# Performance work log

Hardware: AMD Instinct MI355X
Metric: run time of the kernel (lower is better)

## Reference

```python
import jax, jax.numpy as jnp
import numpy as np

COST_MASK = 5.0
COST_DICE = 5.0
COST_BOX = 5.0
COST_GIOU = 2.0


def point_sample(masks, pts):
    # masks: [N, H, W]; pts: [P, 2] with (x, y) in [0, 1].
    # Matches F.grid_sample(bilinear, align_corners=False, padding_mode='zeros')
    N, H, W = masks.shape
    x = pts[:, 0] * W - 0.5
    y = pts[:, 1] * H - 0.5
    x0 = jnp.floor(x)
    y0 = jnp.floor(y)
    wx = x - x0
    wy = y - y0
    x0i = x0.astype(jnp.int32)
    y0i = y0.astype(jnp.int32)

    def gather(yi, xi):
        valid = ((xi >= 0) & (xi < W) & (yi >= 0) & (yi < H)).astype(masks.dtype)
        v = masks[:, jnp.clip(yi, 0, H - 1), jnp.clip(xi, 0, W - 1)]  # [N, P]
        return v * valid

    v00 = gather(y0i, x0i)
    v01 = gather(y0i, x0i + 1)
    v10 = gather(y0i + 1, x0i)
    v11 = gather(y0i + 1, x0i + 1)
    return (v00 * (1 - wy) * (1 - wx) + v01 * (1 - wy) * wx
            + v10 * wy * (1 - wx) + v11 * wy * wx)  # [N, P]


def box_cxcywh_to_xyxy(b):
    cx, cy, w, h = b[..., 0], b[..., 1], b[..., 2], b[..., 3]
    return jnp.stack([cx - 0.5 * w, cy - 0.5 * h, cx + 0.5 * w, cy + 0.5 * h], axis=-1)


def generalized_box_iou(a, b):
    # a: [Q, 4], b: [T, 4] in xyxy
    area_a = (a[:, 2] - a[:, 0]) * (a[:, 3] - a[:, 1])
    area_b = (b[:, 2] - b[:, 0]) * (b[:, 3] - b[:, 1])
    lt = jnp.maximum(a[:, None, :2], b[None, :, :2])
    rb = jnp.minimum(a[:, None, 2:], b[None, :, 2:])
    wh = jnp.clip(rb - lt, 0.0)
    inter = wh[..., 0] * wh[..., 1]
    union = area_a[:, None] + area_b[None, :] - inter
    iou = inter / union
    lt_e = jnp.minimum(a[:, None, :2], b[None, :, :2])
    rb_e = jnp.maximum(a[:, None, 2:], b[None, :, 2:])
    wh_e = jnp.clip(rb_e - lt_e, 0.0)
    area_e = wh_e[..., 0] * wh_e[..., 1]
    return iou - (area_e - union) / area_e


def _cost_one(out_mask, tgt_mask, out_box, tgt_box, pts):
    om = point_sample(out_mask, pts)  # [Q, P] logits
    tm = point_sample(tgt_mask, pts)  # [T, P] binary targets
    P = om.shape[1]
    # batch_sigmoid_ce_loss: BCE(x,1)=softplus(-x), BCE(x,0)=softplus(x)
    pos = jax.nn.softplus(-om)
    neg = jax.nn.softplus(om)
    cost_mask = (jnp.einsum('qp,tp->qt', pos, tm)
                 + jnp.einsum('qp,tp->qt', neg, 1.0 - tm)) / P
    # batch_dice_loss
    s = jax.nn.sigmoid(om)
    numerator = 2.0 * jnp.einsum('qp,tp->qt', s, tm)
    denominator = s.sum(-1)[:, None] + tm.sum(-1)[None, :]
    cost_dice = 1.0 - (numerator + 1.0) / (denominator + 1.0)
    # box costs
    cost_bbox = jnp.abs(out_box[:, None, :] - tgt_box[None, :, :]).sum(-1)
    cost_giou = -generalized_box_iou(box_cxcywh_to_xyxy(out_box),
                                     box_cxcywh_to_xyxy(tgt_box))
    return (COST_MASK * cost_mask + COST_DICE * cost_dice
            + COST_BOX * cost_bbox + COST_GIOU * cost_giou)


def setup_inputs() -> dict:
    key = jax.random.key(0)
    k1, k2, k3, k4, k5 = jax.random.split(key, 5)
    B, Q, T, H, W, P = 2, 300, 300, 256, 256, 12544
    pred_masks = jax.random.normal(k1, (B, Q, H, W), dtype=jnp.float32)
    tgt_masks = (jax.random.uniform(k2, (B, T, H, W)) > 0.5).astype(jnp.float32)
    u = jax.random.uniform(k3, (B, Q, 4), dtype=jnp.float32)
    pred_boxes = jnp.concatenate([0.2 + 0.6 * u[..., :2], 0.05 + 0.25 * u[..., 2:]], axis=-1)
    v = jax.random.uniform(k4, (B, T, 4), dtype=jnp.float32)
    tgt_boxes = jnp.concatenate([0.2 + 0.6 * v[..., :2], 0.05 + 0.25 * v[..., 2:]], axis=-1)
    point_coords = jax.random.uniform(k5, (B, P, 2), dtype=jnp.float32)
    return {"pred_masks": pred_masks, "tgt_masks": tgt_masks,
            "pred_boxes": pred_boxes, "tgt_boxes": tgt_boxes,
            "point_coords": point_coords}


def reference(pred_masks, tgt_masks, pred_boxes, tgt_boxes, point_coords):
    # Batched cost matrix C: [B, Q, T]
    return jax.vmap(_cost_one)(pred_masks, tgt_masks, pred_boxes, tgt_boxes, point_coords)
```

## Files before the change

kernel.cpp:

```cpp
#include <hip/hip_runtime.h>
#include <hip/hip_bf16.h>
#include <math.h>

#define BB 2
#define QQ 300
#define TT 300
#define HH 256
#define WW 256
#define PP 12544
#define NCHUNK 16
#define NSPLIT 14
#define KSPLIT (PP / NSPLIT)
#define KSTEPS (KSPLIT / 64)

typedef __bf16 bf16_t;
typedef bf16_t bf16x8 __attribute__((ext_vector_type(8)));
typedef float floatx4 __attribute__((ext_vector_type(4)));

__device__ inline void gl_lds16(const void* g, void* l) {
    __builtin_amdgcn_global_load_lds(
        (const __attribute__((address_space(1))) unsigned int*)g,
        (__attribute__((address_space(3))) unsigned int*)l, 16, 0, 0);
}

__global__ __launch_bounds__(256) void prep_kernel(const float* __restrict__ pts,
                                                   int4* __restrict__ off,
                                                   float4* __restrict__ wgt,
                                                   int* __restrict__ bkt) {
    int idx = blockIdx.x * 256 + threadIdx.x;
    if (idx >= BB * PP) return;
    float px = pts[idx * 2 + 0];
    float py = pts[idx * 2 + 1];
    float x = px * WW - 0.5f;
    float y = py * HH - 0.5f;
    float x0f = floorf(x), y0f = floorf(y);
    float wx = x - x0f, wy = y - y0f;
    int x0 = (int)x0f, y0 = (int)y0f;
    int x1 = x0 + 1, y1 = y0 + 1;
    float vx0 = (x0 >= 0 && x0 < WW) ? 1.f : 0.f;
    float vx1 = (x1 >= 0 && x1 < WW) ? 1.f : 0.f;
    float vy0 = (y0 >= 0 && y0 < HH) ? 1.f : 0.f;
    float vy1 = (y1 >= 0 && y1 < HH) ? 1.f : 0.f;
    int cx0 = min(max(x0, 0), WW - 1), cx1 = min(max(x1, 0), WW - 1);
    int cy0 = min(max(y0, 0), HH - 1), cy1 = min(max(y1, 0), HH - 1);
    off[idx] = make_int4(cy0 * WW + cx0, cy0 * WW + cx1, cy1 * WW + cx0, cy1 * WW + cx1);
    wgt[idx] = make_float4((1.f - wy) * (1.f - wx) * vy0 * vx0,
                           (1.f - wy) * wx        * vy0 * vx1,
                           wy        * (1.f - wx) * vy1 * vx0,
                           wy        * wx         * vy1 * vx1);
    bkt[idx] = min(max(y0, 0), HH - 2) >> 4;
}

__global__ __launch_bounds__(1024) void sort_kernel(const int4* __restrict__ off,
                                                    const float4* __restrict__ wgt,
                                                    const int* __restrict__ bkt,
                                                    int4* __restrict__ off_s,
                                                    float4* __restrict__ wgt_s,
                                                    int* __restrict__ cs) {
    int b = blockIdx.x;
    int tid = threadIdx.x;
    __shared__ int hist[NCHUNK];
    __shared__ int base_s[NCHUNK];
    if (tid < NCHUNK) hist[tid] = 0;
    __syncthreads();
    for (int p = tid; p < PP; p += 1024) atomicAdd(&hist[bkt[b * PP + p]], 1);
    __syncthreads();
    if (tid == 0) {
        int run = 0;
        for (int i = 0; i < NCHUNK; ++i) { base_s[i] = run; run += hist[i]; }
    }
    __syncthreads();
    if (tid < NCHUNK + 1) cs[b * (NCHUNK + 1) + tid] = (tid < NCHUNK) ? base_s[tid] : PP;
    __syncthreads();
    for (int p = tid; p < PP; p += 1024) {
        int bp = b * PP + p;
        int pos = atomicAdd(&base_s[bkt[bp]], 1);
        off_s[b * PP + pos] = off[bp];
        wgt_s[b * PP + pos] = wgt[bp];
    }
}

__global__ __launch_bounds__(256) void sample_kernel(
    const float* __restrict__ pred_masks, const float* __restrict__ tgt_masks,
    const int4* __restrict__ off_s, const float4* __restrict__ wgt_s,
    const int* __restrict__ cs_g,
    bf16_t* __restrict__ OM, bf16_t* __restrict__ SM, bf16_t* __restrict__ TM,
    float* __restrict__ RS_SP, float* __restrict__ RS_S, float* __restrict__ RS_T) {
    int b = blockIdx.z;
    int m = blockIdx.x;
    int c = blockIdx.y;
    int tid = threadIdx.x;
    int wave = tid >> 6, lane = tid & 63;
    __shared__ __align__(16) float rows[17 * WW];

    bool is_pred = (m < QQ);
    const float* img;
    bf16_t* row0;
    bf16_t* row1 = nullptr;
    if (is_pred) {
        img  = pred_masks + (size_t)(b * QQ + m) * (HH * WW);
        row0 = OM + (size_t)(b * QQ + m) * PP;
        row1 = SM + (size_t)(b * QQ + m) * PP;
    } else {
        int t = m - QQ;
        img  = tgt_masks + (size_t)(b * TT + t) * (HH * WW);
        row0 = TM + (size_t)(b * TT + t) * PP;
    }

    int base = c * 16;
    int nrows = min(17, HH - base);
    const char* gimg = (const char*)(img + base * WW);
    for (int i = wave; i < nrows; i += 4)
        gl_lds16(gimg + i * 1024 + lane * 16, (char*)rows + i * 1024);
    __syncthreads();

    const int4*  offb = off_s + b * PP;
    const float4* wb  = wgt_s + b * PP;
    const int* cs = cs_g + b * (NCHUNK + 1);
    int boff = base * WW;
    int j1 = cs[c + 1];
    float s0 = 0.f, s1 = 0.f;
    for (int j = cs[c] + tid; j < j1; j += 256) {
        int4 o = offb[j];
        float4 w = wb[j];
        float v = w.x * rows[o.x - boff] + w.y * rows[o.y - boff] +
                  w.z * rows[o.z - boff] + w.w * rows[o.w - boff];
        row0[j] = (bf16_t)v;
        if (is_pred) {
            float e = __expf(-fabsf(v));
            float r = 1.f / (1.f + e);
            float sg = (v >= 0.f) ? r : e * r;
            row1[j] = (bf16_t)sg;
            s0 += fmaxf(v, 0.f) + __logf(1.f + e);
            s1 += sg;
        } else {
            s0 += v;
        }
    }
    for (int o = 32; o > 0; o >>= 1) {
        s0 += __shfl_down(s0, o, 64);
        s1 += __shfl_down(s1, o, 64);
    }
    __shared__ float ra[4], rb[4];
    if (lane == 0) { ra[wave] = s0; rb[wave] = s1; }
    __syncthreads();
    if (tid == 0) {
        float t0 = ra[0] + ra[1] + ra[2] + ra[3];
        float t1 = rb[0] + rb[1] + rb[2] + rb[3];
        if (is_pred) {
            atomicAdd(&RS_SP[b * QQ + m], t0);
            atomicAdd(&RS_S[b * QQ + m], t1);
        } else {
            atomicAdd(&RS_T[b * TT + (m - QQ)], t0);
        }
    }
}

__global__ __launch_bounds__(256) void matmul_kernel(
    const bf16_t* __restrict__ OM, const bf16_t* __restrict__ SM, const bf16_t* __restrict__ TM,
    float* __restrict__ A1P, float* __restrict__ A2P) {
    int b = blockIdx.z / NSPLIT;
    int split = blockIdx.z % NSPLIT;
    int m0 = blockIdx.x * 64;
    int n0 = blockIdx.y * 64;
    int tid = threadIdx.x;
    int wave = tid >> 6, lane = tid & 63;
    int lrow = lane & 15, quad = lane >> 4;

    __shared__ __align__(16) bf16_t lds[3 * 64 * 64];

    int k0 = split * KSPLIT;
    int lr8 = lane >> 3;
    int clog = (lane & 7) ^ lr8;

    const char* gp[6];
    unsigned lofs[6];
#pragma unroll
    for (int jj = 0; jj < 6; ++jj) {
        int L = wave + jj * 4;
        int mat = L >> 3, i = L & 7;
        int rb_ = (mat == 2) ? n0 : m0;
        int row = min(rb_ + i * 8 + lr8, (mat == 2) ? (TT - 1) : (QQ - 1));
        const bf16_t* g = (mat == 0) ? OM + (size_t)b * QQ * PP
                        : (mat == 1) ? SM + (size_t)b * QQ * PP
                                     : TM + (size_t)b * TT * PP;
        gp[jj] = (const char*)(g + (size_t)row * PP + k0) + clog * 16;
        lofs[jj] = mat * 4096 + i * 512;
    }

    floatx4 acc1[4] = {{0.f,0.f,0.f,0.f},{0.f,0.f,0.f,0.f},{0.f,0.f,0.f,0.f},{0.f,0.f,0.f,0.f}};
    floatx4 acc2[4] = {{0.f,0.f,0.f,0.f},{0.f,0.f,0.f,0.f},{0.f,0.f,0.f,0.f},{0.f,0.f,0.f,0.f}};

    int ar = wave * 16 + lrow;
    int arx = ar & 7;
    for (int s = 0; s < KSTEPS; ++s) {
#pragma unroll
        for (int jj = 0; jj < 6; ++jj) {
            gl_lds16(gp[jj], lds + lofs[jj]);
            gp[jj] += 128;
        }
        __syncthreads();
#pragma unroll
        for (int kk8 = 0; kk8 <= 4; kk8 += 4) {
            bf16x8 a1 = *(const bf16x8*)(lds + ar * 64 + (((quad + kk8) ^ arx) << 3));
            bf16x8 a2 = *(const bf16x8*)(lds + 4096 + ar * 64 + (((quad + kk8) ^ arx) << 3));
#pragma unroll
            for (int j = 0; j < 4; ++j) {
                int br = j * 16 + lrow;
                bf16x8 bb = *(const bf16x8*)(lds + 8192 + br * 64 + (((quad + kk8) ^ (br & 7)) << 3));
                acc1[j] = __builtin_amdgcn_mfma_f32_16x16x32_bf16(a1, bb, acc1[j], 0, 0, 0);
                acc2[j] = __builtin_amdgcn_mfma_f32_16x16x32_bf16(a2, bb, acc2[j], 0, 0, 0);
            }
        }
        __syncthreads();
    }

    int mrow = m0 + wave * 16 + quad * 4;
    float* o1 = A1P + (size_t)(b * NSPLIT + split) * (QQ * TT);
    float* o2 = A2P + (size_t)(b * NSPLIT + split) * (QQ * TT);
#pragma unroll
    for (int j = 0; j < 4; ++j) {
        int n = n0 + j * 16 + lrow;
        if (n < TT) {
#pragma unroll
            for (int r = 0; r < 4; ++r) {
                int m = mrow + r;
                if (m < QQ) {
                    o1[m * TT + n] = acc1[j][r];
                    o2[m * TT + n] = acc2[j][r];
                }
            }
        }
    }
}

__global__ __launch_bounds__(256) void combine_kernel(
    const float* __restrict__ A1P, const float* __restrict__ A2P,
    const float* __restrict__ RS_SP, const float* __restrict__ RS_S, const float* __restrict__ RS_T,
    const float* __restrict__ pred_boxes, const float* __restrict__ tgt_boxes,
    float* __restrict__ out) {
    int idx = blockIdx.x * 256 + threadIdx.x;
    if (idx >= BB * QQ * TT) return;
    int b = idx / (QQ * TT);
    int r = idx - b * (QQ * TT);
    int q = r / TT;
    int t = r - q * TT;

    float a1 = 0.f, a2 = 0.f;
    for (int s = 0; s < NSPLIT; ++s) {
        a1 += A1P[(size_t)(b * NSPLIT + s) * (QQ * TT) + r];
        a2 += A2P[(size_t)(b * NSPLIT + s) * (QQ * TT) + r];
    }
    float cm = (RS_SP[b * QQ + q] - a1) * (1.0f / (float)PP);
    float cd = 1.f - (2.f * a2 + 1.f) / (RS_S[b * QQ + q] + RS_T[b * TT + t] + 1.f);

    const float* pb = pred_boxes + (size_t)(b * QQ + q) * 4;
    const float* tb = tgt_boxes + (size_t)(b * TT + t) * 4;
    float cb = fabsf(pb[0] - tb[0]) + fabsf(pb[1] - tb[1]) +
               fabsf(pb[2] - tb[2]) + fabsf(pb[3] - tb[3]);

    float ax0 = pb[0] - 0.5f * pb[2], ay0 = pb[1] - 0.5f * pb[3];
    float ax1 = pb[0] + 0.5f * pb[2], ay1 = pb[1] + 0.5f * pb[3];
    float bx0 = tb[0] - 0.5f * tb[2], by0 = tb[1] - 0.5f * tb[3];
    float bx1 = tb[0] + 0.5f * tb[2], by1 = tb[1] + 0.5f * tb[3];
    float area_a = (ax1 - ax0) * (ay1 - ay0);
    float area_b = (bx1 - bx0) * (by1 - by0);
    float iw = fmaxf(fminf(ax1, bx1) - fmaxf(ax0, bx0), 0.f);
    float ih = fmaxf(fminf(ay1, by1) - fmaxf(ay0, by0), 0.f);
    float inter = iw * ih;
    float uni = area_a + area_b - inter;
    float iou = inter / uni;
    float ew = fmaxf(ax1, bx1) - fminf(ax0, bx0);
    float eh = fmaxf(ay1, by1) - fminf(ay0, by0);
    float area_e = ew * eh;
    float giou = iou - (area_e - uni) / area_e;

    out[idx] = 5.f * cm + 5.f * cd + 5.f * cb - 2.f * giou;
}

extern "C" void kernel_launch(void* const* d_in, const int* in_sizes, int n_in,
                              void* d_out, int out_size, void* d_ws, size_t ws_size,
                              hipStream_t stream) {
    const float* pred_masks = (const float*)d_in[0];
    const float* tgt_masks  = (const float*)d_in[1];
    const float* pred_boxes = (const float*)d_in[2];
    const float* tgt_boxes  = (const float*)d_in[3];
    const float* pts        = (const float*)d_in[4];

    char* w = (char*)d_ws;
    auto alloc = [&](size_t bytes) -> char* {
        char* r = w;
        w += (bytes + 255) & ~(size_t)255;
        return r;
    };
    int4*   OFF   = (int4*)  alloc((size_t)BB * PP * sizeof(int4));
    float4* WGT   = (float4*)alloc((size_t)BB * PP * sizeof(float4));
    int*    BKT   = (int*)   alloc((size_t)BB * PP * sizeof(int));
    int4*   OFF_S = (int4*)  alloc((size_t)BB * PP * sizeof(int4));
    float4* WGT_S = (float4*)alloc((size_t)BB * PP * sizeof(float4));
    int*    CS    = (int*)   alloc((size_t)BB * (NCHUNK + 1) * sizeof(int));
    bf16_t* OM    = (bf16_t*)alloc((size_t)BB * QQ * PP * 2);
    bf16_t* SM    = (bf16_t*)alloc((size_t)BB * QQ * PP * 2);
    bf16_t* TM    = (bf16_t*)alloc((size_t)BB * TT * PP * 2);
    float*  RS_SP = (float*) alloc((size_t)BB * QQ * 4);
    float*  RS_S  = (float*) alloc((size_t)BB * QQ * 4);
    float*  RS_T  = (float*) alloc((size_t)BB * TT * 4);
    float*  A1P   = (float*) alloc((size_t)BB * NSPLIT * QQ * TT * 4);
    float*  A2P   = (float*) alloc((size_t)BB * NSPLIT * QQ * TT * 4);

    hipMemsetAsync(RS_SP, 0, (size_t)((char*)A1P - (char*)RS_SP), stream);

    prep_kernel<<<(BB * PP + 255) / 256, 256, 0, stream>>>(pts, OFF, WGT, BKT);
    sort_kernel<<<BB, 1024, 0, stream>>>(OFF, WGT, BKT, OFF_S, WGT_S, CS);
    sample_kernel<<<dim3(QQ + TT, NCHUNK, BB), 256, 0, stream>>>(
        pred_masks, tgt_masks, OFF_S, WGT_S, CS, OM, SM, TM, RS_SP, RS_S, RS_T);
    matmul_kernel<<<dim3(5, 5, BB * NSPLIT), 256, 0, stream>>>(OM, SM, TM, A1P, A2P);
    combine_kernel<<<(BB * QQ * TT + 255) / 256, 256, 0, stream>>>(
        A1P, A2P, RS_SP, RS_S, RS_T, pred_boxes, tgt_boxes, (float*)d_out);
}
```

Baseline: 396.2 us.

## Parallelize point sort, double-buffer sample rows, widen matmul K-split

The single-block-per-batch sort becomes a multi-block histogram, scan and scatter pipeline, removing a serial bottleneck. The sample kernel now covers eight row chunks per block and prefetches the next chunk's rows through registers into a double-buffered LDS tile, overlapping global loads with sampling. The matmul K-split is raised from 14 to 28 when the workspace is large enough, giving more blocks for occupancy at the cost of more partial sums for combine to read. This adds two kernel launches and fewer sample blocks, which may reduce parallelism.

```diff
diff --git a/kernel.cpp b/kernel.cpp
--- a/kernel.cpp
+++ b/kernel.cpp
@@ -9,9 +9,7 @@
 #define WW 256
 #define PP 12544
 #define NCHUNK 16
-#define NSPLIT 14
-#define KSPLIT (PP / NSPLIT)
-#define KSTEPS (KSPLIT / 64)
+#define PBLK (PP / 256)
 
 typedef __bf16 bf16_t;
 typedef bf16_t bf16x8 __attribute__((ext_vector_type(8)));
@@ -23,12 +21,24 @@
         (__attribute__((address_space(3))) unsigned int*)l, 16, 0, 0);
 }
 
+#define CHUNK_BAR() do {                                   \
+    __builtin_amdgcn_sched_barrier(0);                     \
+    asm volatile("s_waitcnt lgkmcnt(0)" ::: "memory");     \
+    __builtin_amdgcn_s_barrier();                          \
+    __builtin_amdgcn_sched_barrier(0);                     \
+} while (0)
+
 __global__ __launch_bounds__(256) void prep_kernel(const float* __restrict__ pts,
                                                    int4* __restrict__ off,
                                                    float4* __restrict__ wgt,
-                                                   int* __restrict__ bkt) {
-    int idx = blockIdx.x * 256 + threadIdx.x;
-    if (idx >= BB * PP) return;
+                                                   int* __restrict__ bkt,
+                                                   int* __restrict__ hist) {
+    __shared__ int lh[NCHUNK];
+    int tid = threadIdx.x;
+    if (tid < NCHUNK) lh[tid] = 0;
+    __syncthreads();
+    int idx = blockIdx.x * 256 + tid;
+    int b = blockIdx.x / PBLK;
     float px = pts[idx * 2 + 0];
     float py = pts[idx * 2 + 1];
     float x = px * WW - 0.5f;
@@ -48,36 +58,64 @@
                            (1.f - wy) * wx        * vy0 * vx1,
                            wy        * (1.f - wx) * vy1 * vx0,
                            wy        * wx         * vy1 * vx1);
-    bkt[idx] = min(max(y0, 0), HH - 2) >> 4;
-}
-
-__global__ __launch_bounds__(1024) void sort_kernel(const int4* __restrict__ off,
-                                                    const float4* __restrict__ wgt,
-                                                    const int* __restrict__ bkt,
-                                                    int4* __restrict__ off_s,
-                                                    float4* __restrict__ wgt_s,
-                                                    int* __restrict__ cs) {
-    int b = blockIdx.x;
+    int k = min(max(y0, 0), HH - 2) >> 4;
+    bkt[idx] = k;
+    atomicAdd(&lh[k], 1);
+    __syncthreads();
+    if (tid < NCHUNK && lh[tid] > 0) atomicAdd(&hist[b * NCHUNK + tid], lh[tid]);
+}
+
+__global__ void scan_kernel(const int* __restrict__ hist, int* __restrict__ cs,
+                            int* __restrict__ ctr) {
+    int b = threadIdx.x;
+    if (b < BB) {
+        int run = 0;
+        for (int k = 0; k < NCHUNK; ++k) {
+            cs[b * (NCHUNK + 1) + k] = run;
+            ctr[b * NCHUNK + k] = run;
+            run += hist[b * NCHUNK + k];
+        }
+        cs[b * (NCHUNK + 1) + NCHUNK] = run;
+    }
+}
+
+__global__ __launch_bounds__(256) void scatter_kernel(const int4* __restrict__ off,
+                                                      const float4* __restrict__ wgt,
+                                                      const int* __restrict__ bkt,
+                                                      int* __restrict__ ctr,
+                                                      int4* __restrict__ off_s,
+                                                      float4* __restrict__ wgt_s) {
+    __shared__ int lh[NCHUNK];
+    __shared__ int lbase[NCHUNK];
     int tid = threadIdx.x;
-    __shared__ int hist[NCHUNK];
-    __shared__ int base_s[NCHUNK];
-    if (tid < NCHUNK) hist[tid] = 0;
-    __syncthreads();
-    for (int p = tid; p < PP; p += 1024) atomicAdd(&hist[bkt[b * PP + p]], 1);
-    __syncthreads();
-    if (tid == 0) {
-        int run = 0;
-        for (int i = 0; i < NCHUNK; ++i) { base_s[i] = run; run += hist[i]; }
-    }
-    __syncthreads();
-    if (tid < NCHUNK + 1) cs[b * (NCHUNK + 1) + tid] = (tid < NCHUNK) ? base_s[tid] : PP;
-    __syncthreads();
-    for (int p = tid; p < PP; p += 1024) {
-        int bp = b * PP + p;
-        int pos = atomicAdd(&base_s[bkt[bp]], 1);
-        off_s[b * PP + pos] = off[bp];
-        wgt_s[b * PP + pos] = wgt[bp];
-    }
+    if (tid < NCHUNK) lh[tid] = 0;
+    __syncthreads();
+    int idx = blockIdx.x * 256 + tid;
+    int b = blockIdx.x / PBLK;
+    int k = bkt[idx];
+    int rank = atomicAdd(&lh[k], 1);
+    __syncthreads();
+    if (tid < NCHUNK) lbase[tid] = (lh[tid] > 0) ? atomicAdd(&ctr[b * NCHUNK + tid], lh[tid]) : 0;
+    __syncthreads();
+    int pos = lbase[k] + rank;
+    off_s[b * PP + pos] = off[idx];
+    wgt_s[b * PP + pos] = wgt[idx];
+}
+
+__device__ __forceinline__ void load_rows(const float* __restrict__ img, int c,
+                                          int wave, int lane, float4* r) {
+    const float4* src = (const float4*)(img + c * 16 * WW) + lane;
+#pragma unroll
+    for (int k = 0; k < 4; ++k) r[k] = src[(wave + 4 * k) * (WW / 4)];
+    if (wave == 0 && c < 15) r[4] = src[16 * (WW / 4)];
+}
+
+__device__ __forceinline__ void write_rows(float* __restrict__ buf, int c,
+                                           int wave, int lane, const float4* r) {
+    float4* d = (float4*)buf + lane;
+#pragma unroll
+    for (int k = 0; k < 4; ++k) d[(wave + 4 * k) * (WW / 4)] = r[k];
+    if (wave == 0 && c < 15) d[16 * (WW / 4)] = r[4];
 }
 
 __global__ __launch_bounds__(256) void sample_kernel(
@@ -88,10 +126,11 @@
     float* __restrict__ RS_SP, float* __restrict__ RS_S, float* __restrict__ RS_T) {
     int b = blockIdx.z;
     int m = blockIdx.x;
-    int c = blockIdx.y;
+    int half = blockIdx.y;
     int tid = threadIdx.x;
     int wave = tid >> 6, lane = tid & 63;
-    __shared__ __align__(16) float rows[17 * WW];
+    __shared__ __align__(16) float rows[2][17 * WW];
+    __shared__ float ra_[4], rb_[4];
 
     bool is_pred = (m < QQ);
     const float* img;
@@ -107,46 +146,62 @@
         row0 = TM + (size_t)(b * TT + t) * PP;
     }
 
-    int base = c * 16;
-    int nrows = min(17, HH - base);
-    const char* gimg = (const char*)(img + base * WW);
-    for (int i = wave; i < nrows; i += 4)
-        gl_lds16(gimg + i * 1024 + lane * 16, (char*)rows + i * 1024);
-    __syncthreads();
-
-    const int4*  offb = off_s + b * PP;
-    const float4* wb  = wgt_s + b * PP;
-    const int* cs = cs_g + b * (NCHUNK + 1);
-    int boff = base * WW;
-    int j1 = cs[c + 1];
+    const int4*   offb = off_s + b * PP;
+    const float4* wb   = wgt_s + b * PP;
+    const int*    cs   = cs_g + b * (NCHUNK + 1);
+    int c0 = half * 8;
+
+    float4 rA[5], rB[5];
+    load_rows(img, c0, wave, lane, rA);
+    write_rows(rows[0], c0, wave, lane, rA);
+    load_rows(img, c0 + 1, wave, lane, rB);
+    CHUNK_BAR();
+
     float s0 = 0.f, s1 = 0.f;
-    for (int j = cs[c] + tid; j < j1; j += 256) {
-        int4 o = offb[j];
-        float4 w = wb[j];
-        float v = w.x * rows[o.x - boff] + w.y * rows[o.y - boff] +
-                  w.z * rows[o.z - boff] + w.w * rows[o.w - boff];
-        row0[j] = (bf16_t)v;
-        if (is_pred) {
-            float e = __expf(-fabsf(v));
-            float r = 1.f / (1.f + e);
-            float sg = (v >= 0.f) ? r : e * r;
-            row1[j] = (bf16_t)sg;
-            s0 += fmaxf(v, 0.f) + __logf(1.f + e);
-            s1 += sg;
-        } else {
-            s0 += v;
-        }
-    }
+#pragma unroll
+    for (int i = 0; i < 8; ++i) {
+        const int c = c0 + i;
+        const float* lrows = rows[i & 1];
+        int boff = c * 16 * WW;
+        int j1 = cs[c + 1];
+        for (int j = cs[c] + tid; j < j1; j += 256) {
+            int4 o = offb[j];
+            float4 w = wb[j];
+            float v = w.x * lrows[o.x - boff] + w.y * lrows[o.y - boff] +
+                      w.z * lrows[o.z - boff] + w.w * lrows[o.w - boff];
+            row0[j] = (bf16_t)v;
+            if (is_pred) {
+                float e = __expf(-fabsf(v));
+                float r = 1.f / (1.f + e);
+                float sg = (v >= 0.f) ? r : e * r;
+                row1[j] = (bf16_t)sg;
+                s0 += fmaxf(v, 0.f) + __logf(1.f + e);
+                s1 += sg;
+            } else {
+                s0 += v;
+            }
+        }
+        if (i < 7) {
+            if ((i & 1) == 0) {
+                write_rows(rows[1], c + 1, wave, lane, rB);
+                if (i < 6) load_rows(img, c + 2, wave, lane, rA);
+            } else {
+                write_rows(rows[0], c + 1, wave, lane, rA);
+                if (i < 6) load_rows(img, c + 2, wave, lane, rB);
+            }
+            CHUNK_BAR();
+        }
+    }
+
     for (int o = 32; o > 0; o >>= 1) {
         s0 += __shfl_down(s0, o, 64);
         s1 += __shfl_down(s1, o, 64);
     }
-    __shared__ float ra[4], rb[4];
-    if (lane == 0) { ra[wave] = s0; rb[wave] = s1; }
+    if (lane == 0) { ra_[wave] = s0; rb_[wave] = s1; }
     __syncthreads();
     if (tid == 0) {
-        float t0 = ra[0] + ra[1] + ra[2] + ra[3];
-        float t1 = rb[0] + rb[1] + rb[2] + rb[3];
+        float t0 = ra_[0] + ra_[1] + ra_[2] + ra_[3];
+        float t1 = rb_[0] + rb_[1] + rb_[2] + rb_[3];
         if (is_pred) {
             atomicAdd(&RS_SP[b * QQ + m], t0);
             atomicAdd(&RS_S[b * QQ + m], t1);
@@ -156,11 +211,15 @@
     }
 }
 
+template<int NS>
 __global__ __launch_bounds__(256) void matmul_kernel(
     const bf16_t* __restrict__ OM, const bf16_t* __restrict__ SM, const bf16_t* __restrict__ TM,
     float* __restrict__ A1P, float* __restrict__ A2P) {
-    int b = blockIdx.z / NSPLIT;
-    int split = blockIdx.z % NSPLIT;
+    constexpr int KSP = PP / NS;
+    constexpr int KST = KSP / 64;
+    static_assert(KSP % 64 == 0, "K split must be a multiple of 64");
+    int b = blockIdx.z / NS;
+    int split = blockIdx.z % NS;
     int m0 = blockIdx.x * 64;
     int n0 = blockIdx.y * 64;
     int tid = threadIdx.x;
@@ -169,7 +228,7 @@
 
     __shared__ __align__(16) bf16_t lds[3 * 64 * 64];
 
-    int k0 = split * KSPLIT;
+    int k0 = split * KSP;
     int lr8 = lane >> 3;
     int clog = (lane & 7) ^ lr8;
 
@@ -193,7 +252,7 @@
 
     int ar = wave * 16 + lrow;
     int arx = ar & 7;
-    for (int s = 0; s < KSTEPS; ++s) {
+    for (int s = 0; s < KST; ++s) {
 #pragma unroll
         for (int jj = 0; jj < 6; ++jj) {
             gl_lds16(gp[jj], lds + lofs[jj]);
@@ -216,24 +275,25 @@
     }
 
     int mrow = m0 + wave * 16 + quad * 4;
-    float* o1 = A1P + (size_t)(b * NSPLIT + split) * (QQ * TT);
-    float* o2 = A2P + (size_t)(b * NSPLIT + split) * (QQ * TT);
+    float* o1 = A1P + (size_t)(b * NS + split) * (QQ * TT);
+    float* o2 = A2P + (size_t)(b * NS + split) * (QQ * TT);
 #pragma unroll
     for (int j = 0; j < 4; ++j) {
         int n = n0 + j * 16 + lrow;
         if (n < TT) {
 #pragma unroll
             for (int r = 0; r < 4; ++r) {
-                int m = mrow + r;
-                if (m < QQ) {
-                    o1[m * TT + n] = acc1[j][r];
-                    o2[m * TT + n] = acc2[j][r];
+                int mm = mrow + r;
+                if (mm < QQ) {
+                    o1[mm * TT + n] = acc1[j][r];
+                    o2[mm * TT + n] = acc2[j][r];
                 }
             }
         }
     }
 }
 
+template<int NS>
 __global__ __launch_bounds__(256) void combine_kernel(
     const float* __restrict__ A1P, const float* __restrict__ A2P,
     const float* __restrict__ RS_SP, const float* __restrict__ RS_S, const float* __restrict__ RS_T,
@@ -247,9 +307,9 @@
     int t = r - q * TT;
 
     float a1 = 0.f, a2 = 0.f;
-    for (int s = 0; s < NSPLIT; ++s) {
-        a1 += A1P[(size_t)(b * NSPLIT + s) * (QQ * TT) + r];
-        a2 += A2P[(size_t)(b * NSPLIT + s) * (QQ * TT) + r];
+    for (int s = 0; s < NS; ++s) {
+        a1 += A1P[(size_t)(b * NS + s) * (QQ * TT) + r];
+        a2 += A2P[(size_t)(b * NS + s) * (QQ * TT) + r];
     }
     float cm = (RS_SP[b * QQ + q] - a1) * (1.0f / (float)PP);
     float cd = 1.f - (2.f * a2 + 1.f) / (RS_S[b * QQ + q] + RS_T[b * TT + t] + 1.f);
@@ -305,16 +365,29 @@
     float*  RS_SP = (float*) alloc((size_t)BB * QQ * 4);
     float*  RS_S  = (float*) alloc((size_t)BB * QQ * 4);
     float*  RS_T  = (float*) alloc((size_t)BB * TT * 4);
-    float*  A1P   = (float*) alloc((size_t)BB * NSPLIT * QQ * TT * 4);
-    float*  A2P   = (float*) alloc((size_t)BB * NSPLIT * QQ * TT * 4);
+    int*    HIST  = (int*)   alloc((size_t)BB * NCHUNK * sizeof(int));
+    int*    CTR   = (int*)   alloc((size_t)BB * NCHUNK * sizeof(int));
+
+    size_t used = (size_t)(w - (char*)d_ws);
+    size_t per_arr28 = (size_t)BB * 28 * QQ * TT * 4;
+    int NS = (ws_size >= used + 2 * per_arr28 + 4096) ? 28 : 14;
+    float* A1P = (float*)alloc((size_t)BB * NS * QQ * TT * 4);
+    float* A2P = (float*)alloc((size_t)BB * NS * QQ * TT * 4);
 
     hipMemsetAsync(RS_SP, 0, (size_t)((char*)A1P - (char*)RS_SP), stream);
 
-    prep_kernel<<<(BB * PP + 255) / 256, 256, 0, stream>>>(pts, OFF, WGT, BKT);
-    sort_kernel<<<BB, 1024, 0, stream>>>(OFF, WGT, BKT, OFF_S, WGT_S, CS);
-    sample_kernel<<<dim3(QQ + TT, NCHUNK, BB), 256, 0, stream>>>(
+    prep_kernel<<<BB * PBLK, 256, 0, stream>>>(pts, OFF, WGT, BKT, HIST);
+    scan_kernel<<<1, 64, 0, stream>>>(HIST, CS, CTR);
+    scatter_kernel<<<BB * PBLK, 256, 0, stream>>>(OFF, WGT, BKT, CTR, OFF_S, WGT_S);
+    sample_kernel<<<dim3(QQ + TT, 2, BB), 256, 0, stream>>>(
         pred_masks, tgt_masks, OFF_S, WGT_S, CS, OM, SM, TM, RS_SP, RS_S, RS_T);
-    matmul_kernel<<<dim3(5, 5, BB * NSPLIT), 256, 0, stream>>>(OM, SM, TM, A1P, A2P);
-    combine_kernel<<<(BB * QQ * TT + 255) / 256, 256, 0, stream>>>(
-        A1P, A2P, RS_SP, RS_S, RS_T, pred_boxes, tgt_boxes, (float*)d_out);
-}
+    if (NS == 28) {
+        matmul_kernel<28><<<dim3(5, 5, BB * 28), 256, 0, stream>>>(OM, SM, TM, A1P, A2P);
+        combine_kernel<28><<<(BB * QQ * TT + 255) / 256, 256, 0, stream>>>(
+            A1P, A2P, RS_SP, RS_S, RS_T, pred_boxes, tgt_boxes, (float*)d_out);
+    } else {
+        matmul_kernel<14><<<dim3(5, 5, BB * 14), 256, 0, stream>>>(OM, SM, TM, A1P, A2P);
+        combine_kernel<14><<<(BB * QQ * TT + 255) / 256, 256, 0, stream>>>(
+            A1P, A2P, RS_SP, RS_S, RS_T, pred_boxes, tgt_boxes, (float*)d_out);
+    }
+}
```

Result: slower. 487.9 us (+23.1%).
